# Performance work log

Hardware: AMD Instinct MI355X
Metric: run time of the kernel (lower is better)

Reference implementation:

```python
import jax, jax.numpy as jnp
import numpy as np

BN_EPS = 1e-5

def _conv(x, W, b, stride, pad):
    # x: [B,C,H,W], W: [O,I,kh,kw]
    y = jax.lax.conv_general_dilated(
        x, W, window_strides=(stride, stride),
        padding=[(pad, pad), (pad, pad)],
        dimension_numbers=('NCHW', 'OIHW', 'NCHW'))
    return y + b[None, :, None, None]

def _bn(x, gamma, beta, mean, var):
    inv = gamma * jax.lax.rsqrt(var + BN_EPS)
    return x * inv[None, :, None, None] + (beta - mean * inv)[None, :, None, None]

def _haar_cD(x):
    # pywt.dwt2(x, 'haar') diagonal detail over last two axes (even H,W):
    # cD[i,j] = (x[2i,2j] - x[2i,2j+1] - x[2i+1,2j] + x[2i+1,2j+1]) / 2
    a = x[..., 0::2, 0::2]
    b = x[..., 0::2, 1::2]
    c = x[..., 1::2, 0::2]
    d = x[..., 1::2, 1::2]
    return (a - b - c + d) * 0.5

def setup_inputs() -> dict:
    key = jax.random.key(0)
    ks = jax.random.split(key, 20)
    B = 8192
    f32 = jnp.float32
    inp = {
        'x':   jax.random.normal(ks[0], (B, 3, 32, 32), dtype=f32),
        # conv1: 3 -> 32, k5 s2 p2
        'w1':  jax.random.normal(ks[1], (32, 3, 5, 5), dtype=f32) * 0.05,
        'b1':  jnp.zeros((32,), f32),
        'g1':  jnp.ones((32,), f32),
        'be1': jnp.zeros((32,), f32),
        'm1':  jax.random.normal(ks[2], (32,), dtype=f32) * 0.1,
        'v1':  jax.random.uniform(ks[3], (32,), dtype=f32, minval=0.5, maxval=1.5),
        # conv2: 32 -> 64, k3 s2 p1
        'w2':  jax.random.normal(ks[4], (64, 32, 3, 3), dtype=f32) * 0.05,
        'b2':  jnp.zeros((64,), f32),
        'g2':  jnp.ones((64,), f32),
        'be2': jnp.zeros((64,), f32),
        'm2':  jax.random.normal(ks[5], (64,), dtype=f32) * 0.1,
        'v2':  jax.random.uniform(ks[6], (64,), dtype=f32, minval=0.5, maxval=1.5),
        # attention conv: 64 -> 1, k1
        'wa':  jax.random.normal(ks[7], (1, 64, 1, 1), dtype=f32) * 0.1,
        'ba':  jnp.zeros((1,), f32),
        # decoder linears (torch Linear layout: [out, in])
        'wd1': jax.random.normal(ks[8], (512, 64 * 8 * 8), dtype=f32) * 0.02,
        'bd1': jnp.zeros((512,), f32),
        'wd2': jax.random.normal(ks[9], (128, 512), dtype=f32) * 0.04,
        'bd2': jnp.zeros((128,), f32),
    }
    return inp

def reference(x, w1, b1, g1, be1, m1, v1, w2, b2, g2, be2, m2, v2,
              wa, ba, wd1, bd1, wd2, bd2):
    # wavelet_conv stem
    h = jax.nn.relu(_bn(_conv(x, w1, b1, 2, 2), g1, be1, m1, v1))   # [B,32,16,16]
    feat = jax.nn.relu(_bn(_conv(h, w2, b2, 2, 1), g2, be2, m2, v2))  # [B,64,8,8]
    # Haar DWT diagonal-detail gate (detached in the original)
    cD = jax.lax.stop_gradient(_haar_cD(feat))                        # [B,64,4,4]
    cD_up = jnp.repeat(jnp.repeat(cD, 2, axis=-2), 2, axis=-1)        # [B,64,8,8]
    feat = feat * cD_up
    # attention gate
    attn = jax.nn.sigmoid(_conv(feat, wa, ba, 1, 0))                  # [B,1,8,8]
    feat = feat * attn
    # decode
    f = feat.reshape(feat.shape[0], -1)                               # [B,4096]
    h1 = jax.nn.relu(f @ wd1.T + bd1)                                  # [B,512]
    return jax.nn.sigmoid(h1 @ wd2.T + bd2)                            # [B,128]
```

## Files before the change

kernel.cpp:

```cpp
#include <hip/hip_runtime.h>
#include <hip/hip_bf16.h>

typedef __bf16 bf16x8 __attribute__((ext_vector_type(8)));
typedef __bf16 bf16x4 __attribute__((ext_vector_type(4)));
typedef float f32x4 __attribute__((ext_vector_type(4)));

#define BN_EPS 1e-5f

__device__ __forceinline__ void gl_lds16(const __bf16* g, __bf16* l) {
    __builtin_amdgcn_global_load_lds(
        (const __attribute__((address_space(1))) unsigned int*)g,
        (__attribute__((address_space(3))) unsigned int*)l,
        16, 0, 0);
}

__global__ __launch_bounds__(256) void wd1p_kernel(const float* __restrict__ wd1, __bf16* __restrict__ o) {
    __shared__ float t2[64][65];
    const int n = blockIdx.x;
    const int tid = threadIdx.x;
    const float* src = wd1 + (size_t)n * 4096;
    #pragma unroll
    for (int r = 0; r < 16; ++r) {
        int j = r * 256 + tid;
        t2[j & 63][j >> 6] = src[j];
    }
    __syncthreads();
    __bf16* dst = o + (size_t)n * 4096;
    #pragma unroll
    for (int r = 0; r < 16; ++r) {
        int t = r * 256 + tid;
        dst[t] = (__bf16)t2[t >> 6][t & 63];
    }
}

__global__ void prep_kernel(const float* __restrict__ wd2, const float* __restrict__ w1,
                            const float* __restrict__ w2,
                            __bf16* __restrict__ wd2o, __bf16* __restrict__ w1o,
                            __bf16* __restrict__ w2o) {
    int i = blockIdx.x * 256 + threadIdx.x;
    if (i < 65536) { wd2o[i] = (__bf16)wd2[i]; return; }
    i -= 65536;
    if (i < 4096) {
        int oc = i >> 7, rem = i & 127;
        int ot = rem >> 3, j = rem & 7;
        float v = 0.f;
        if (ot < 15 && j < 5) {
            int ic = ot / 5, ky = ot % 5;
            v = w1[((oc * 3 + ic) * 5 + ky) * 5 + j];
        }
        w1o[i] = (__bf16)v;
        return;
    }
    i -= 4096;
    if (i < 18432) {
        int oc = i / 288, rem = i % 288;
        int tap = rem / 32, ic = rem % 32;
        w2o[i] = (__bf16)w2[(oc * 32 + ic) * 9 + tap];
    }
}

__global__ __launch_bounds__(256, 5) void conv_fused_kernel(
    const float* __restrict__ x,
    const __bf16* __restrict__ w1r, const float* __restrict__ b1,
    const float* __restrict__ g1, const float* __restrict__ be1,
    const float* __restrict__ m1, const float* __restrict__ v1,
    const __bf16* __restrict__ w2r, const float* __restrict__ b2,
    const float* __restrict__ g2, const float* __restrict__ be2,
    const float* __restrict__ m2, const float* __restrict__ v2,
    const float* __restrict__ wa, const float* __restrict__ ba,
    __bf16* __restrict__ f)
{
    __shared__ __align__(16) __bf16 xsb[3 * 36 * 40];
    __shared__ __align__(16) char  ubuf[23120];
    __bf16* hsf  = (__bf16*)ubuf;
    float*  feat = (float*)ubuf;
    float*  cds  = (float*)(ubuf + 16384);
    float*  atn  = (float*)(ubuf + 20480);

    const int b    = blockIdx.x;
    const int tid  = threadIdx.x;
    const int lane = tid & 63;
    const int wave = tid >> 6;
    const int lo   = lane >> 4;
    const int ln   = lane & 15;

    {
        bf16x8 z = {};
        for (int i = tid; i < 540; i += 256) *(bf16x8*)&xsb[i * 8] = z;
        if (tid < 132) {
            int pi = tid >> 2, ch = tid & 3;
            int pix = (pi < 17) ? pi : (pi - 16) * 17;
            *(bf16x8*)&hsf[pix * 40 + ch * 8] = z;
        }
    }
    __syncthreads();

    {
        const float4* xb = (const float4*)(x + (size_t)b * 3072);
        #pragma unroll
        for (int r = 0; r < 3; ++r) {
            int c = r * 256 + tid;
            int plane = c >> 8, rem = c & 255;
            int row = rem >> 3, c4 = rem & 7;
            float4 v = xb[c];
            bf16x4 h;
            h[0] = (__bf16)v.x; h[1] = (__bf16)v.y; h[2] = (__bf16)v.z; h[3] = (__bf16)v.w;
            *(bf16x4*)&xsb[plane * 1440 + (row + 2) * 40 + 4 + c4 * 4] = h;
        }
    }

    bf16x8 bw1[2][4];
    #pragma unroll
    for (int nt = 0; nt < 2; ++nt)
        #pragma unroll
        for (int s = 0; s < 4; ++s)
            bw1[nt][s] = *(const bf16x8*)(w1r + (nt * 16 + ln) * 128 + (s * 4 + lo) * 8);
    __syncthreads();

    f32x4 c1[4][2] = {};
    const unsigned int* xw = (const unsigned int*)xsb;
    #pragma unroll
    for (int s = 0; s < 4; ++s) {
        const int o  = s * 4 + lo;
        const int ic = (o * 205) >> 10;
        const int ky = o - ic * 5;
        const bool dummy = (o == 15);
        const int icc = dummy ? 2 : ic;
        #pragma unroll
        for (int mt = 0; mt < 4; ++mt) {
            const int oy  = wave * 4 + mt;
            const int row = dummy ? 35 : (2 * oy + ky);
            const int dw  = icc * 720 + row * 20 + ln + 1;
            union { unsigned int u[4]; bf16x8 v; } fa;
            fa.u[0] = xw[dw]; fa.u[1] = xw[dw + 1]; fa.u[2] = xw[dw + 2]; fa.u[3] = 0;
            #pragma unroll
            for (int nt = 0; nt < 2; ++nt)
                c1[mt][nt] = __builtin_amdgcn_mfma_f32_16x16x32_bf16(fa.v, bw1[nt][s], c1[mt][nt], 0, 0, 0);
        }
    }

    #pragma unroll
    for (int nt = 0; nt < 2; ++nt) {
        const int oc  = nt * 16 + ln;
        const float inv = g1[oc] * rsqrtf(v1[oc] + BN_EPS);
        const float bb  = be1[oc] + (b1[oc] - m1[oc]) * inv;
        #pragma unroll
        for (int mt = 0; mt < 4; ++mt) {
            const int hy = wave * 4 + mt + 1;
            #pragma unroll
            for (int r = 0; r < 4; ++r) {
                const int hx = lo * 4 + r + 1;
                hsf[(hy * 17 + hx) * 40 + oc] = (__bf16)fmaxf(c1[mt][nt][r] * inv + bb, 0.f);
            }
        }
    }

    const int wm = wave >> 1, wn = wave & 1;
    bf16x8 bw2[2][9];
    #pragma unroll
    for (int nt = 0; nt < 2; ++nt) {
        const __bf16* wp = w2r + (wn * 32 + nt * 16 + ln) * 288 + lo * 8;
        #pragma unroll
        for (int ks = 0; ks < 9; ++ks)
            bw2[nt][ks] = *(const bf16x8*)(wp + ks * 32);
    }
    __syncthreads();

    f32x4 c2[2][2] = {};
    {
        int pixbase[2];
        #pragma unroll
        for (int mt = 0; mt < 2; ++mt) {
            int p = wm * 32 + mt * 16 + ln;
            int qy = p >> 3, qx = p & 7;
            pixbase[mt] = (2 * qy * 17 + 2 * qx) * 40 + lo * 8;
        }
        #pragma unroll
        for (int ks = 0; ks < 9; ++ks) {
            const int ty = ks / 3, tx = ks % 3;
            bf16x8 af[2];
            #pragma unroll
            for (int mt = 0; mt < 2; ++mt)
                af[mt] = *(const bf16x8*)&hsf[pixbase[mt] + (ty * 17 + tx) * 40];
            #pragma unroll
            for (int mt = 0; mt < 2; ++mt)
                #pragma unroll
                for (int nt = 0; nt < 2; ++nt)
                    c2[mt][nt] = __builtin_amdgcn_mfma_f32_16x16x32_bf16(af[mt], bw2[nt][ks], c2[mt][nt], 0, 0, 0);
        }
    }
    __syncthreads();

    #pragma unroll
    for (int nt = 0; nt < 2; ++nt) {
        const int oc  = wn * 32 + nt * 16 + ln;
        const float inv = g2[oc] * rsqrtf(v2[oc] + BN_EPS);
        const float bb  = be2[oc] + (b2[oc] - m2[oc]) * inv;
        #pragma unroll
        for (int mt = 0; mt < 2; ++mt)
            #pragma unroll
            for (int r = 0; r < 4; ++r) {
                const int p = wm * 32 + mt * 16 + lo * 4 + r;
                feat[oc * 64 + p] = fmaxf(c2[mt][nt][r] * inv + bb, 0.f);
            }
    }
    __syncthreads();

    #pragma unroll
    for (int r = 0; r < 4; ++r) {
        int idx = tid * 4 + r;
        int c = idx >> 4, yx = idx & 15;
        int y = yx >> 2, xx = yx & 3;
        float aa = feat[c * 64 + (2 * y) * 8 + 2 * xx];
        float bb = feat[c * 64 + (2 * y) * 8 + 2 * xx + 1];
        float cc = feat[c * 64 + (2 * y + 1) * 8 + 2 * xx];
        float dd = feat[c * 64 + (2 * y + 1) * 8 + 2 * xx + 1];
        cds[c * 16 + yx] = 0.5f * (aa - bb - cc + dd);
    }
    __syncthreads();

    const int q  = tid & 63;
    const int g  = wave;
    const int qy2 = q >> 3, qx2 = q & 7;
    const int qq = (qy2 >> 1) * 4 + (qx2 >> 1);
    float a2[16];
    float part = 0.f;
    #pragma unroll
    for (int j = 0; j < 16; ++j) {
        int oc = g * 16 + j;
        float v = feat[oc * 64 + q] * cds[oc * 16 + qq];
        a2[j] = v;
        part += v * wa[oc];
    }
    atn[g * 64 + q] = part;
    __syncthreads();
    float s2  = atn[q] + atn[64 + q] + atn[128 + q] + atn[192 + q] + ba[0];
    float sig = 1.f / (1.f + __expf(-s2));

    bf16x8 fo0, fo1;
    #pragma unroll
    for (int j = 0; j < 8; ++j) {
        fo0[j] = (__bf16)(a2[j] * sig);
        fo1[j] = (__bf16)(a2[j + 8] * sig);
    }
    __bf16* fb = f + (size_t)b * 4096 + q * 64 + g * 16;
    *(bf16x8*)fb = fo0;
    *(bf16x8*)(fb + 8) = fo1;
}

__global__ __launch_bounds__(256, 4) void gemm1_split_kernel(
    const __bf16* __restrict__ A, const __bf16* __restrict__ B,
    float* __restrict__ P)
{
    const int K = 4096, NOUT = 512, KH = 2048;
    __shared__ __align__(16) __bf16 As[64][64];
    __shared__ __align__(16) __bf16 Bs[128][64];
    const int tid  = threadIdx.x;
    const int lane = tid & 63;
    const int wave = tid >> 6;
    const int lo = lane >> 4, ln = lane & 15;
    const int m0 = blockIdx.x * 64, n0 = blockIdx.y * 128;
    const int ks0 = blockIdx.z * KH;
    const int sw = ln & 7;
    f32x4 acc[4][2] = {};
    for (int k0 = ks0; k0 < ks0 + KH; k0 += 64) {
        #pragma unroll
        for (int r = 0; r < 2; ++r) {
            int i = r * 256 + tid;
            int row = i >> 3, cs = i & 7;
            gl_lds16(A + (size_t)(m0 + row) * K + k0 + (cs ^ (row & 7)) * 8, &As[0][0] + i * 8);
        }
        #pragma unroll
        for (int r = 0; r < 4; ++r) {
            int i = r * 256 + tid;
            int row = i >> 3, cs = i & 7;
            gl_lds16(B + (size_t)(n0 + row) * K + k0 + (cs ^ (row & 7)) * 8, &Bs[0][0] + i * 8);
        }
        __syncthreads();
        #pragma unroll
        for (int s = 0; s < 2; ++s) {
            const int c = s * 4 + lo;
            const int slot = (c ^ sw) * 8;
            bf16x8 af[4], bfr[2];
            #pragma unroll
            for (int mt = 0; mt < 4; ++mt)
                af[mt] = *(const bf16x8*)(&As[mt * 16 + ln][slot]);
            #pragma unroll
            for (int nt = 0; nt < 2; ++nt)
                bfr[nt] = *(const bf16x8*)(&Bs[wave * 32 + nt * 16 + ln][slot]);
            #pragma unroll
            for (int mt = 0; mt < 4; ++mt)
                #pragma unroll
                for (int nt = 0; nt < 2; ++nt)
                    acc[mt][nt] = __builtin_amdgcn_mfma_f32_16x16x32_bf16(af[mt], bfr[nt], acc[mt][nt], 0, 0, 0);
        }
        __syncthreads();
    }
    float* Pp = P + (size_t)blockIdx.z * 8192 * 512;
    #pragma unroll
    for (int mt = 0; mt < 4; ++mt)
        #pragma unroll
        for (int nt = 0; nt < 2; ++nt)
            #pragma unroll
            for (int r = 0; r < 4; ++r) {
                int m = m0 + mt * 16 + lo * 4 + r;
                int n = n0 + wave * 32 + nt * 16 + ln;
                Pp[(size_t)m * NOUT + n] = acc[mt][nt][r];
            }
}

__global__ __launch_bounds__(256) void reduce1_kernel(
    const float* __restrict__ P, const float* __restrict__ bias, __bf16* __restrict__ h1)
{
    const size_t HALF = (size_t)8192 * 512;
    size_t i4 = ((size_t)blockIdx.x * 256 + threadIdx.x) * 4;
    f32x4 p0 = *(const f32x4*)(P + i4);
    f32x4 p1 = *(const f32x4*)(P + HALF + i4);
    f32x4 bv = *(const f32x4*)(bias + (i4 & 511));
    bf16x4 o;
    #pragma unroll
    for (int j = 0; j < 4; ++j)
        o[j] = (__bf16)fmaxf(p0[j] + p1[j] + bv[j], 0.f);
    *(bf16x4*)(h1 + i4) = o;
}

__global__ __launch_bounds__(256) void gemm1_kernel(
    const __bf16* __restrict__ A, const __bf16* __restrict__ B,
    const float* __restrict__ bias, __bf16* __restrict__ C)
{
    const int K = 4096, NOUT = 512;
    __shared__ __align__(16) __bf16 As[64][64];
    __shared__ __align__(16) __bf16 Bs[128][64];
    const int tid  = threadIdx.x;
    const int lane = tid & 63;
    const int wave = tid >> 6;
    const int lo = lane >> 4, ln = lane & 15;
    const int m0 = blockIdx.x * 64, n0 = blockIdx.y * 128;
    const int sw = ln & 7;
    f32x4 acc[4][2] = {};
    for (int k0 = 0; k0 < K; k0 += 64) {
        #pragma unroll
        for (int r = 0; r < 2; ++r) {
            int i = r * 256 + tid;
            int row = i >> 3, cs = i & 7;
            gl_lds16(A + (size_t)(m0 + row) * K + k0 + (cs ^ (row & 7)) * 8, &As[0][0] + i * 8);
        }
        #pragma unroll
        for (int r = 0; r < 4; ++r) {
            int i = r * 256 + tid;
            int row = i >> 3, cs = i & 7;
            gl_lds16(B + (size_t)(n0 + row) * K + k0 + (cs ^ (row & 7)) * 8, &Bs[0][0] + i * 8);
        }
        __syncthreads();
        #pragma unroll
        for (int s = 0; s < 2; ++s) {
            const int c = s * 4 + lo;
            const int slot = (c ^ sw) * 8;
            bf16x8 af[4], bfr[2];
            #pragma unroll
            for (int mt = 0; mt < 4; ++mt)
                af[mt] = *(const bf16x8*)(&As[mt * 16 + ln][slot]);
            #pragma unroll
            for (int nt = 0; nt < 2; ++nt)
                bfr[nt] = *(const bf16x8*)(&Bs[wave * 32 + nt * 16 + ln][slot]);
            #pragma unroll
            for (int mt = 0; mt < 4; ++mt)
                #pragma unroll
                for (int nt = 0; nt < 2; ++nt)
                    acc[mt][nt] = __builtin_amdgcn_mfma_f32_16x16x32_bf16(af[mt], bfr[nt], acc[mt][nt], 0, 0, 0);
        }
        __syncthreads();
    }
    #pragma unroll
    for (int mt = 0; mt < 4; ++mt)
        #pragma unroll
        for (int nt = 0; nt < 2; ++nt)
            #pragma unroll
            for (int r = 0; r < 4; ++r) {
                int m = m0 + mt * 16 + lo * 4 + r;
                int n = n0 + wave * 32 + nt * 16 + ln;
                float v = acc[mt][nt][r] + bias[n];
                C[(size_t)m * NOUT + n] = (__bf16)fmaxf(v, 0.f);
            }
}

__global__ __launch_bounds__(256, 4) void gemm2_kernel(
    const __bf16* __restrict__ A, const __bf16* __restrict__ B,
    const float* __restrict__ bias, float* __restrict__ Out)
{
    const int K = 512, NOUT = 128;
    __shared__ __align__(16) __bf16 As[32][64];
    __shared__ __align__(16) __bf16 Bs[128][64];
    const int tid  = threadIdx.x;
    const int lane = tid & 63;
    const int wave = tid >> 6;
    const int lo = lane >> 4, ln = lane & 15;
    const int m0 = blockIdx.x * 32;
    const int sw = ln & 7;
    f32x4 acc[2][2] = {};
    for (int k0 = 0; k0 < K; k0 += 64) {
        {
            int i = tid;
            int row = i >> 3, cs = i & 7;
            gl_lds16(A + (size_t)(m0 + row) * K + k0 + (cs ^ (row & 7)) * 8, &As[0][0] + i * 8);
        }
        #pragma unroll
        for (int r = 0; r < 4; ++r) {
            int i = r * 256 + tid;
            int row = i >> 3, cs = i & 7;
            gl_lds16(B + (size_t)row * K + k0 + (cs ^ (row & 7)) * 8, &Bs[0][0] + i * 8);
        }
        __syncthreads();
        #pragma unroll
        for (int s = 0; s < 2; ++s) {
            const int c = s * 4 + lo;
            const int slot = (c ^ sw) * 8;
            bf16x8 af[2], bfr[2];
            #pragma unroll
            for (int mt = 0; mt < 2; ++mt)
                af[mt] = *(const bf16x8*)(&As[mt * 16 + ln][slot]);
            #pragma unroll
            for (int nt = 0; nt < 2; ++nt)
                bfr[nt] = *(const bf16x8*)(&Bs[wave * 32 + nt * 16 + ln][slot]);
            #pragma unroll
            for (int mt = 0; mt < 2; ++mt)
                #pragma unroll
                for (int nt = 0; nt < 2; ++nt)
                    acc[mt][nt] = __builtin_amdgcn_mfma_f32_16x16x32_bf16(af[mt], bfr[nt], acc[mt][nt], 0, 0, 0);
        }
        __syncthreads();
    }
    #pragma unroll
    for (int mt = 0; mt < 2; ++mt)
        #pragma unroll
        for (int nt = 0; nt < 2; ++nt)
            #pragma unroll
            for (int r = 0; r < 4; ++r) {
                int m = m0 + mt * 16 + lo * 4 + r;
                int n = wave * 32 + nt * 16 + ln;
                float v = acc[mt][nt][r] + bias[n];
                Out[(size_t)m * NOUT + n] = 1.f / (1.f + __expf(-v));
            }
}

extern "C" void kernel_launch(void* const* d_in, const int* in_sizes, int n_in,
                              void* d_out, int out_size, void* d_ws, size_t ws_size,
                              hipStream_t stream)
{
    const float* x   = (const float*)d_in[0];
    const float* w1  = (const float*)d_in[1];
    const float* b1  = (const float*)d_in[2];
    const float* g1  = (const float*)d_in[3];
    const float* be1 = (const float*)d_in[4];
    const float* m1  = (const float*)d_in[5];
    const float* v1  = (const float*)d_in[6];
    const float* w2  = (const float*)d_in[7];
    const float* b2  = (const float*)d_in[8];
    const float* g2  = (const float*)d_in[9];
    const float* be2 = (const float*)d_in[10];
    const float* m2  = (const float*)d_in[11];
    const float* v2  = (const float*)d_in[12];
    const float* wa  = (const float*)d_in[13];
    const float* ba  = (const float*)d_in[14];
    const float* wd1 = (const float*)d_in[15];
    const float* bd1 = (const float*)d_in[16];
    const float* wd2 = (const float*)d_in[17];
    const float* bd2 = (const float*)d_in[18];

    char* ws = (char*)d_ws;
    const size_t SZ_F  = 67108864;
    const size_t SZ_P  = 33554432;
    const size_t SZ_H1 = 8388608;
    const bool use_split = ws_size >= (SZ_F + SZ_P + SZ_H1 + 4194304 + 131072 + 65536 + 8192);

    __bf16* f_bf = (__bf16*)ws;
    float*  P;
    __bf16* h1_bf;
    char* tail;
    if (use_split) {
        P      = (float*)(ws + SZ_F);
        h1_bf  = (__bf16*)(ws + SZ_F + SZ_P);
        tail   = ws + SZ_F + SZ_P + SZ_H1;
    } else {
        P      = nullptr;
        h1_bf  = (__bf16*)(ws + SZ_F);
        tail   = ws + SZ_F + SZ_H1;
    }
    __bf16* wd1_bf = (__bf16*)tail;
    __bf16* wd2_bf = (__bf16*)(tail + 4194304);
    __bf16* w2r_bf = (__bf16*)(tail + 4194304 + 131072);
    __bf16* w1r_bf = (__bf16*)(tail + 4194304 + 131072 + 65536);

    prep_kernel<<<344, 256, 0, stream>>>(wd2, w1, w2, wd2_bf, w1r_bf, w2r_bf);
    wd1p_kernel<<<512, 256, 0, stream>>>(wd1, wd1_bf);

    conv_fused_kernel<<<8192, 256, 0, stream>>>(x, w1r_bf, b1, g1, be1, m1, v1,
                                                w2r_bf, b2, g2, be2, m2, v2, wa, ba, f_bf);

    if (use_split) {
        dim3 g3(128, 4, 2);
        gemm1_split_kernel<<<g3, 256, 0, stream>>>(f_bf, wd1_bf, P);
        reduce1_kernel<<<4096, 256, 0, stream>>>(P, bd1, h1_bf);
    } else {
        dim3 g3(128, 4);
        gemm1_kernel<<<g3, 256, 0, stream>>>(f_bf, wd1_bf, bd1, h1_bf);
    }

    gemm2_kernel<<<256, 256, 0, stream>>>(h1_bf, wd2_bf, bd2, (float*)d_out);
}
```

Before: 311.9 us.

## Transpose conv MFMA outputs for vectorized LDS stores and swizzle GEMM block order

```diff
diff --git a/kernel.cpp b/kernel.cpp
--- a/kernel.cpp
+++ b/kernel.cpp
@@ -74,8 +74,8 @@
     __shared__ __align__(16) char  ubuf[23120];
     __bf16* hsf  = (__bf16*)ubuf;
     float*  feat = (float*)ubuf;
-    float*  cds  = (float*)(ubuf + 16384);
-    float*  atn  = (float*)(ubuf + 20480);
+    float*  cds  = (float*)(ubuf + 17408);
+    float*  atn  = (float*)(ubuf + 21760);
 
     const int b    = blockIdx.x;
     const int tid  = threadIdx.x;
@@ -135,23 +135,33 @@
             fa.u[0] = xw[dw]; fa.u[1] = xw[dw + 1]; fa.u[2] = xw[dw + 2]; fa.u[3] = 0;
             #pragma unroll
             for (int nt = 0; nt < 2; ++nt)
-                c1[mt][nt] = __builtin_amdgcn_mfma_f32_16x16x32_bf16(fa.v, bw1[nt][s], c1[mt][nt], 0, 0, 0);
+                c1[mt][nt] = __builtin_amdgcn_mfma_f32_16x16x32_bf16(bw1[nt][s], fa.v, c1[mt][nt], 0, 0, 0);
         }
     }
 
     #pragma unroll
     for (int nt = 0; nt < 2; ++nt) {
-        const int oc  = nt * 16 + ln;
-        const float inv = g1[oc] * rsqrtf(v1[oc] + BN_EPS);
-        const float bb  = be1[oc] + (b1[oc] - m1[oc]) * inv;
+        const int ocb = nt * 16 + lo * 4;
+        const f32x4 gv  = *(const f32x4*)(g1 + ocb);
+        const f32x4 vv  = *(const f32x4*)(v1 + ocb);
+        const f32x4 bev = *(const f32x4*)(be1 + ocb);
+        const f32x4 b1v = *(const f32x4*)(b1 + ocb);
+        const f32x4 mv  = *(const f32x4*)(m1 + ocb);
+        f32x4 inv, bb;
+        #pragma unroll
+        for (int r = 0; r < 4; ++r) {
+            inv[r] = gv[r] * rsqrtf(vv[r] + BN_EPS);
+            bb[r]  = bev[r] + (b1v[r] - mv[r]) * inv[r];
+        }
         #pragma unroll
         for (int mt = 0; mt < 4; ++mt) {
             const int hy = wave * 4 + mt + 1;
-            #pragma unroll
-            for (int r = 0; r < 4; ++r) {
-                const int hx = lo * 4 + r + 1;
-                hsf[(hy * 17 + hx) * 40 + oc] = (__bf16)fmaxf(c1[mt][nt][r] * inv + bb, 0.f);
-            }
+            const int hx = ln + 1;
+            bf16x4 h;
+            #pragma unroll
+            for (int r = 0; r < 4; ++r)
+                h[r] = (__bf16)fmaxf(c1[mt][nt][r] * inv[r] + bb[r], 0.f);
+            *(bf16x4*)&hsf[(hy * 17 + hx) * 40 + ocb] = h;
         }
     }
 
@@ -186,51 +196,68 @@
             for (int mt = 0; mt < 2; ++mt)
                 #pragma unroll
                 for (int nt = 0; nt < 2; ++nt)
-                    c2[mt][nt] = __builtin_amdgcn_mfma_f32_16x16x32_bf16(af[mt], bw2[nt][ks], c2[mt][nt], 0, 0, 0);
+                    c2[mt][nt] = __builtin_amdgcn_mfma_f32_16x16x32_bf16(bw2[nt][ks], af[mt], c2[mt][nt], 0, 0, 0);
         }
     }
     __syncthreads();
 
     #pragma unroll
     for (int nt = 0; nt < 2; ++nt) {
-        const int oc  = wn * 32 + nt * 16 + ln;
-        const float inv = g2[oc] * rsqrtf(v2[oc] + BN_EPS);
-        const float bb  = be2[oc] + (b2[oc] - m2[oc]) * inv;
-        #pragma unroll
-        for (int mt = 0; mt < 2; ++mt)
-            #pragma unroll
-            for (int r = 0; r < 4; ++r) {
-                const int p = wm * 32 + mt * 16 + lo * 4 + r;
-                feat[oc * 64 + p] = fmaxf(c2[mt][nt][r] * inv + bb, 0.f);
-            }
-    }
-    __syncthreads();
-
-    #pragma unroll
-    for (int r = 0; r < 4; ++r) {
-        int idx = tid * 4 + r;
-        int c = idx >> 4, yx = idx & 15;
-        int y = yx >> 2, xx = yx & 3;
-        float aa = feat[c * 64 + (2 * y) * 8 + 2 * xx];
-        float bb = feat[c * 64 + (2 * y) * 8 + 2 * xx + 1];
-        float cc = feat[c * 64 + (2 * y + 1) * 8 + 2 * xx];
-        float dd = feat[c * 64 + (2 * y + 1) * 8 + 2 * xx + 1];
-        cds[c * 16 + yx] = 0.5f * (aa - bb - cc + dd);
-    }
-    __syncthreads();
-
-    const int q  = tid & 63;
+        const int ocb = wn * 32 + nt * 16 + lo * 4;
+        const f32x4 gv  = *(const f32x4*)(g2 + ocb);
+        const f32x4 vv  = *(const f32x4*)(v2 + ocb);
+        const f32x4 bev = *(const f32x4*)(be2 + ocb);
+        const f32x4 b2v = *(const f32x4*)(b2 + ocb);
+        const f32x4 mv  = *(const f32x4*)(m2 + ocb);
+        f32x4 inv, bb;
+        #pragma unroll
+        for (int r = 0; r < 4; ++r) {
+            inv[r] = gv[r] * rsqrtf(vv[r] + BN_EPS);
+            bb[r]  = bev[r] + (b2v[r] - mv[r]) * inv[r];
+        }
+        #pragma unroll
+        for (int mt = 0; mt < 2; ++mt) {
+            const int p = wm * 32 + mt * 16 + ln;
+            f32x4 o;
+            #pragma unroll
+            for (int r = 0; r < 4; ++r)
+                o[r] = fmaxf(c2[mt][nt][r] * inv[r] + bb[r], 0.f);
+            *(f32x4*)&feat[p * 68 + ocb] = o;
+        }
+    }
+    __syncthreads();
+
+    {
+        const int c  = tid & 63;
+        const int g4 = tid >> 6;
+        #pragma unroll
+        for (int r = 0; r < 4; ++r) {
+            const int pa = (16 * g4 + 2 * r) * 68 + c;
+            float aa  = feat[pa];
+            float bb2 = feat[pa + 68];
+            float cc  = feat[pa + 8 * 68];
+            float dd  = feat[pa + 9 * 68];
+            cds[c * 17 + g4 * 4 + r] = 0.5f * (aa - bb2 - cc + dd);
+        }
+    }
+    __syncthreads();
+
+    const int q  = lane;
     const int g  = wave;
-    const int qy2 = q >> 3, qx2 = q & 7;
-    const int qq = (qy2 >> 1) * 4 + (qx2 >> 1);
+    const int qq = (q >> 4) * 4 + ((q & 7) >> 1);
     float a2[16];
     float part = 0.f;
     #pragma unroll
-    for (int j = 0; j < 16; ++j) {
-        int oc = g * 16 + j;
-        float v = feat[oc * 64 + q] * cds[oc * 16 + qq];
-        a2[j] = v;
-        part += v * wa[oc];
+    for (int j4 = 0; j4 < 4; ++j4) {
+        const f32x4 fv = *(const f32x4*)&feat[q * 68 + g * 16 + j4 * 4];
+        const f32x4 wv = *(const f32x4*)(wa + g * 16 + j4 * 4);
+        #pragma unroll
+        for (int r = 0; r < 4; ++r) {
+            const int j = j4 * 4 + r;
+            float v = fv[r] * cds[(g * 16 + j) * 17 + qq];
+            a2[j] = v;
+            part += v * wv[r];
+        }
     }
     atn[g * 64 + q] = part;
     __syncthreads();
@@ -259,8 +286,12 @@
     const int lane = tid & 63;
     const int wave = tid >> 6;
     const int lo = lane >> 4, ln = lane & 15;
-    const int m0 = blockIdx.x * 64, n0 = blockIdx.y * 128;
-    const int ks0 = blockIdx.z * KH;
+    const int bid = blockIdx.x;
+    const int swz = (bid & 7) * 128 + (bid >> 3);
+    const int n0  = (swz & 3) * 128;
+    const int zz  = (swz >> 2) & 1;
+    const int m0  = (swz >> 3) * 64;
+    const int ks0 = zz * KH;
     const int sw = ln & 7;
     f32x4 acc[4][2] = {};
     for (int k0 = ks0; k0 < ks0 + KH; k0 += 64) {
@@ -296,7 +327,7 @@
         }
         __syncthreads();
     }
-    float* Pp = P + (size_t)blockIdx.z * 8192 * 512;
+    float* Pp = P + (size_t)zz * 8192 * 512;
     #pragma unroll
     for (int mt = 0; mt < 4; ++mt)
         #pragma unroll
@@ -335,7 +366,10 @@
     const int lane = tid & 63;
     const int wave = tid >> 6;
     const int lo = lane >> 4, ln = lane & 15;
-    const int m0 = blockIdx.x * 64, n0 = blockIdx.y * 128;
+    const int bid = blockIdx.x;
+    const int swz = (bid & 7) * 64 + (bid >> 3);
+    const int n0  = (swz & 3) * 128;
+    const int m0  = (swz >> 2) * 64;
     const int sw = ln & 7;
     f32x4 acc[4][2] = {};
     for (int k0 = 0; k0 < K; k0 += 64) {
@@ -498,12 +532,10 @@
                                                 w2r_bf, b2, g2, be2, m2, v2, wa, ba, f_bf);
 
     if (use_split) {
-        dim3 g3(128, 4, 2);
-        gemm1_split_kernel<<<g3, 256, 0, stream>>>(f_bf, wd1_bf, P);
+        gemm1_split_kernel<<<1024, 256, 0, stream>>>(f_bf, wd1_bf, P);
         reduce1_kernel<<<4096, 256, 0, stream>>>(P, bd1, h1_bf);
     } else {
-        dim3 g3(128, 4);
-        gemm1_kernel<<<g3, 256, 0, stream>>>(f_bf, wd1_bf, bd1, h1_bf);
+        gemm1_kernel<<<512, 256, 0, stream>>>(f_bf, wd1_bf, bd1, h1_bf);
     }
 
     gemm2_kernel<<<256, 256, 0, stream>>>(h1_bf, wd2_bf, bd2, (float*)d_out);
```

Measured after the change: 319.7 us. 2.5% more time.
